# Kernel optimization log

Hardware: AMD Instinct MI355X
Metric: run time of the kernel (lower is better)

Reference implementation:

```python
import jax, jax.numpy as jnp
import numpy as np

N = 4096      # nodes
F = 512       # nfeat
D = 64        # nhid per head
H = 8         # nheads
C = 40        # nclass
ALPHA = 0.2   # leakyrelu slope
NEG = -1e9    # mask value (finite for bf16/fp16 safety; exp -> 0)
EDGE_P = 0.004


def setup_inputs() -> dict:
    key = jax.random.key(0)
    ks = jax.random.split(key, 8)
    x = jax.random.normal(ks[0], (N, F), jnp.float32)
    adj = jax.random.uniform(ks[1], (N, N)) < EDGE_P
    adj = adj | jnp.eye(N, dtype=bool)  # self-loops: every softmax row valid
    init = lambda k, shape, fan: jax.random.normal(k, shape, jnp.float32) / np.sqrt(fan)
    W1 = init(ks[2], (H, F, D), F)        # per-head tran.weight^T
    a1_src = init(ks[3], (H, D), D)       # att1 (j / source term)
    a1_dst = init(ks[4], (H, D), D)       # att2 (i / destination term)
    W2 = init(ks[5], (H * D, C), H * D)   # output head tran
    a2_src = init(ks[6], (C,), C)
    a2_dst = init(ks[7], (C,), C)
    return dict(x=x, adj=adj, W1=W1, a1_src=a1_src, a1_dst=a1_dst,
                W2=W2, a2_src=a2_src, a2_dst=a2_dst)


def reference(x, adj, W1, a1_src, a1_dst, W2, a2_src, a2_dst):
    # ---- layer 1: H heads in parallel (dropout = identity in eval) ----
    h = jnp.einsum('nf,hfd->hnd', x, W1)              # [H,N,D]
    si = jnp.einsum('hnd,hd->hn', h, a1_dst)          # att2(h): i term
    sj = jnp.einsum('hnd,hd->hn', h, a1_src)          # att1(h): j term
    e = jax.nn.leaky_relu(si[:, :, None] + sj[:, None, :], ALPHA)  # [H,N,N]
    e = jnp.where(adj[None], e, NEG)                  # mask non-edges
    p = jax.nn.softmax(e, axis=-1)                    # softmax over neighbors j
    out = jnp.einsum('hij,hjd->hid', p, h)            # [H,N,D]
    # torch.cat(heads, dim=1) -> [N, H*D] with heads contiguous
    x2 = jax.nn.elu(jnp.transpose(out, (1, 0, 2)).reshape(N, H * D))
    # ---- output attention head ----
    h2 = x2 @ W2                                      # [N,C]
    e2 = jax.nn.leaky_relu((h2 @ a2_dst)[:, None] + (h2 @ a2_src)[None, :], ALPHA)
    e2 = jnp.where(adj, e2, NEG)
    p2 = jax.nn.softmax(e2, axis=-1)
    return p2 @ h2                                    # [N,C]
```

## Files before the change

kernel.cpp:

```cpp
#include <hip/hip_runtime.h>

#define NN 4096
#define FF 512
#define DD 64
#define HH 8
#define CC 40
#define HD (HH * DD)
#define CP 64
#define MAXDEG 128
#define ALPHA 0.2f

#define BM 64
#define BN 64
#define BK 16
#define SK 2
#define KH (FF / SK)
#define SK2 8
#define KH2 (FF / SK2)

__device__ __forceinline__ float bf2f(unsigned short u) {
    union { unsigned int i; float f; } v;
    v.i = ((unsigned int)u) << 16;
    return v.f;
}

__device__ __forceinline__ float wave_sum(float v) {
    #pragma unroll
    for (int off = 32; off; off >>= 1) v += __shfl_xor(v, off, 64);
    return v;
}

__device__ __forceinline__ float wave_max(float v) {
    #pragma unroll
    for (int off = 32; off; off >>= 1) v = fmaxf(v, __shfl_xor(v, off, 64));
    return v;
}

__device__ __forceinline__ float read_f(const void* src, int i, int isBf16) {
    if (isBf16) return bf2f(((const unsigned short*)src)[i]);
    return ((const float*)src)[i];
}

__global__ __launch_bounds__(64) void init_flags(int* __restrict__ flagA,
                                                 int* __restrict__ flagF) {
    if (threadIdx.x == 0) { *flagA = 1; *flagF = 1; }
}

__global__ __launch_bounds__(64) void sniff_adj(const unsigned char* __restrict__ adj,
                                                int* __restrict__ flagA) {
    int i = blockIdx.x * 64 + threadIdx.x;
    if (adj[(size_t)i * (NN + 1)] == 0) *flagA = 0;
}

__global__ __launch_bounds__(256) void sniff_fdt(const unsigned int* __restrict__ xw,
                                                 int* __restrict__ flagF) {
    int bad = 0;
    #pragma unroll
    for (int q = 0; q < 4; q++) {
        unsigned int w = xw[(blockIdx.x * 4 + q) * 256 + threadIdx.x];
        unsigned int e0 = (w >> 7) & 0xffu;
        unsigned int e1 = (w >> 23) & 0xffu;
        if (e0 >= 0x90u || e1 >= 0x90u) bad = 1;
    }
    if (bad) *flagF = 0;
}

__global__ __launch_bounds__(256) void cvt_all(const void* __restrict__ x,
                                               const void* __restrict__ W1,
                                               const void* __restrict__ W2,
                                               const void* __restrict__ a1s,
                                               const void* __restrict__ a1d,
                                               const void* __restrict__ a2s,
                                               const void* __restrict__ a2d,
                                               float* __restrict__ xf,
                                               float* __restrict__ W1t,
                                               float* __restrict__ W2p,
                                               float* __restrict__ a1sf,
                                               float* __restrict__ a1df,
                                               float* __restrict__ a2sf,
                                               float* __restrict__ a2df,
                                               const int* __restrict__ flagF) {
    int i = blockIdx.x * 256 + threadIdx.x;
    int bf = *flagF;
    const int nX = NN * FF;
    const int nW1 = HH * FF * DD;
    const int nW2p = HD * CP;
    const int nA1 = HD;
    if (i < nX) { xf[i] = read_f(x, i, bf); return; }
    i -= nX;
    if (i < nW1) {
        int hd = i / (FF * DD);
        int rem = i % (FF * DD);
        int f = rem / DD, d = rem % DD;
        W1t[f * HD + hd * DD + d] = read_f(W1, i, bf);
        return;
    }
    i -= nW1;
    if (i < nW2p) {
        int k = i / CP, c = i % CP;
        W2p[i] = (c < CC) ? read_f(W2, k * CC + c, bf) : 0.f;
        return;
    }
    i -= nW2p;
    if (i < nA1) { a1sf[i] = read_f(a1s, i, bf); return; }
    i -= nA1;
    if (i < nA1) { a1df[i] = read_f(a1d, i, bf); return; }
    i -= nA1;
    if (i < CC) { a2sf[i] = read_f(a2s, i, bf); return; }
    i -= CC;
    if (i < CC) { a2df[i] = read_f(a2d, i, bf); return; }
}

__global__ __launch_bounds__(256) void build_nbr(const unsigned char* __restrict__ adj,
                                                 const int* __restrict__ flagA,
                                                 int* __restrict__ nbr,
                                                 int* __restrict__ deg) {
    int i = blockIdx.x;
    __shared__ int cnt;
    if (threadIdx.x == 0) cnt = 0;
    __syncthreads();
    if (*flagA) {
        uint4 v = ((const uint4*)(adj + (size_t)i * NN))[threadIdx.x];
        unsigned int u[4] = { v.x, v.y, v.z, v.w };
        int base = threadIdx.x * 16;
        #pragma unroll
        for (int q = 0; q < 4; q++) {
            #pragma unroll
            for (int b = 0; b < 4; b++) {
                if ((u[q] >> (8 * b)) & 0xffu) {
                    int p = atomicAdd(&cnt, 1);
                    if (p < MAXDEG) nbr[(size_t)i * MAXDEG + p] = base + q * 4 + b;
                }
            }
        }
    } else {
        const int4* row = (const int4*)((const int*)adj + (size_t)i * NN);
        #pragma unroll
        for (int q = 0; q < 4; q++) {
            int idx4 = q * 256 + threadIdx.x;
            int4 v = row[idx4];
            int base = idx4 * 4;
            if (v.x) { int p = atomicAdd(&cnt, 1); if (p < MAXDEG) nbr[(size_t)i * MAXDEG + p] = base; }
            if (v.y) { int p = atomicAdd(&cnt, 1); if (p < MAXDEG) nbr[(size_t)i * MAXDEG + p] = base + 1; }
            if (v.z) { int p = atomicAdd(&cnt, 1); if (p < MAXDEG) nbr[(size_t)i * MAXDEG + p] = base + 2; }
            if (v.w) { int p = atomicAdd(&cnt, 1); if (p < MAXDEG) nbr[(size_t)i * MAXDEG + p] = base + 3; }
        }
    }
    __syncthreads();
    if (threadIdx.x == 0) deg[i] = min(cnt, MAXDEG);
}

template <int KHs, int Nb>
__device__ __forceinline__ void gemm_body(const float* __restrict__ Ap,
                                          const float* __restrict__ Bp,
                                          float* __restrict__ Co,
                                          int tid, int bm) {
    __shared__ float As[BK][BM + 4];
    __shared__ float Bs[BK][BN + 4];
    int tm = tid >> 4, tn = tid & 15;
    int m0 = tm * 4, n0 = tn * 4;
    int ar = tid >> 2, ak = (tid & 3) * 4;
    int bk = tid >> 4, bq = (tid & 15) * 4;

    float acc[4][4];
    #pragma unroll
    for (int r = 0; r < 4; r++)
        #pragma unroll
        for (int c = 0; c < 4; c++) acc[r][c] = 0.f;

    const float* Ar = Ap + (size_t)ar * FF;
    float4 av = *(const float4*)(Ar + ak);
    float4 bv = *(const float4*)(Bp + (size_t)bk * Nb + bq);

    for (int k0 = 0; k0 < KHs; k0 += BK) {
        __syncthreads();
        As[ak + 0][ar] = av.x;
        As[ak + 1][ar] = av.y;
        As[ak + 2][ar] = av.z;
        As[ak + 3][ar] = av.w;
        *(float4*)&Bs[bk][bq] = bv;
        __syncthreads();

        int kn = (k0 + BK < KHs) ? k0 + BK : k0;
        av = *(const float4*)(Ar + kn + ak);
        bv = *(const float4*)(Bp + (size_t)(kn + bk) * Nb + bq);

        #pragma unroll
        for (int k = 0; k < BK; k++) {
            float4 a = *(const float4*)&As[k][m0];
            float4 b = *(const float4*)&Bs[k][n0];
            acc[0][0] = fmaf(a.x, b.x, acc[0][0]);
            acc[0][1] = fmaf(a.x, b.y, acc[0][1]);
            acc[0][2] = fmaf(a.x, b.z, acc[0][2]);
            acc[0][3] = fmaf(a.x, b.w, acc[0][3]);
            acc[1][0] = fmaf(a.y, b.x, acc[1][0]);
            acc[1][1] = fmaf(a.y, b.y, acc[1][1]);
            acc[1][2] = fmaf(a.y, b.z, acc[1][2]);
            acc[1][3] = fmaf(a.y, b.w, acc[1][3]);
            acc[2][0] = fmaf(a.z, b.x, acc[2][0]);
            acc[2][1] = fmaf(a.z, b.y, acc[2][1]);
            acc[2][2] = fmaf(a.z, b.z, acc[2][2]);
            acc[2][3] = fmaf(a.z, b.w, acc[2][3]);
            acc[3][0] = fmaf(a.w, b.x, acc[3][0]);
            acc[3][1] = fmaf(a.w, b.y, acc[3][1]);
            acc[3][2] = fmaf(a.w, b.z, acc[3][2]);
            acc[3][3] = fmaf(a.w, b.w, acc[3][3]);
        }
    }

    #pragma unroll
    for (int r = 0; r < 4; r++) {
        float4 v = make_float4(acc[r][0], acc[r][1], acc[r][2], acc[r][3]);
        *(float4*)(Co + (size_t)(bm * BM + m0 + r) * Nb + n0) = v;
    }
}

__global__ __launch_bounds__(256) void l1_gemm(const float* __restrict__ xf,
                                               const float* __restrict__ W1t,
                                               float* __restrict__ Cp) {
    int bm = blockIdx.x, bn = blockIdx.y, sk = blockIdx.z;
    gemm_body<KH, HD>(xf + (size_t)bm * BM * FF + sk * KH,
                      W1t + (size_t)(sk * KH) * HD + bn * BN,
                      Cp + (size_t)sk * NN * HD + bn * BN,
                      threadIdx.x, bm);
}

__global__ __launch_bounds__(256) void l1_post(const float* __restrict__ Cp,
                                               const float* __restrict__ a1sf,
                                               const float* __restrict__ a1df,
                                               float* __restrict__ h,
                                               float* __restrict__ si,
                                               float* __restrict__ sj) {
    int n = blockIdx.x, tid = threadIdx.x;
    #pragma unroll
    for (int q = 0; q < 2; q++) {
        int t = q * 256 + tid;
        float v = Cp[(size_t)n * HD + t] + Cp[(size_t)NN * HD + (size_t)n * HD + t];
        h[(size_t)n * HD + t] = v;
        int hd = t >> 6;
        float pd = wave_sum(v * a1df[t]);
        float ps = wave_sum(v * a1sf[t]);
        if ((t & 63) == 0) {
            si[hd * NN + n] = pd;
            sj[hd * NN + n] = ps;
        }
    }
}

__global__ __launch_bounds__(512) void l1_attn(const int* __restrict__ nbr,
                                               const int* __restrict__ deg,
                                               const float* __restrict__ h,
                                               const float* __restrict__ si,
                                               const float* __restrict__ sj,
                                               float* __restrict__ x2) {
    int i = blockIdx.x;
    int tid = threadIdx.x;
    int hd = tid >> 6, lane = tid & 63;
    int d = deg[i];
    __shared__ int js[MAXDEG];
    __shared__ float wls[HH][MAXDEG];
    for (int k = tid; k < d; k += 512) js[k] = nbr[(size_t)i * MAXDEG + k];
    __syncthreads();

    float sii = si[hd * NN + i];
    const float* sjh = sj + (size_t)hd * NN;
    float m = -1e30f;
    for (int k = lane; k < d; k += 64) {
        float sc = sii + sjh[js[k]];
        sc = sc > 0.f ? sc : ALPHA * sc;
        wls[hd][k] = sc;
        m = fmaxf(m, sc);
    }
    m = wave_max(m);
    float s = 0.f;
    for (int k = lane; k < d; k += 64) {
        float e = expf(wls[hd][k] - m);
        wls[hd][k] = e;
        s += e;
    }
    s = fmaxf(wave_sum(s), 1e-30f);

    float acc = 0.f;
    int k = 0;
    for (; k + 4 <= d; k += 4) {
        float v0 = h[(size_t)js[k] * HD + tid];
        float v1 = h[(size_t)js[k + 1] * HD + tid];
        float v2 = h[(size_t)js[k + 2] * HD + tid];
        float v3 = h[(size_t)js[k + 3] * HD + tid];
        acc = fmaf(wls[hd][k], v0, acc);
        acc = fmaf(wls[hd][k + 1], v1, acc);
        acc = fmaf(wls[hd][k + 2], v2, acc);
        acc = fmaf(wls[hd][k + 3], v3, acc);
    }
    for (; k < d; k++)
        acc = fmaf(wls[hd][k], h[(size_t)js[k] * HD + tid], acc);
    acc /= s;
    float r = acc > 0.f ? acc : expm1f(acc);
    x2[(size_t)i * HD + tid] = r;
}

__global__ __launch_bounds__(256) void l2_gemm(const float* __restrict__ x2,
                                               const float* __restrict__ W2p,
                                               float* __restrict__ Cp2) {
    int bm = blockIdx.x, sk = blockIdx.z;
    gemm_body<KH2, CP>(x2 + (size_t)bm * BM * FF + sk * KH2,
                       W2p + (size_t)(sk * KH2) * CP,
                       Cp2 + (size_t)sk * NN * CP,
                       threadIdx.x, bm);
}

__global__ __launch_bounds__(64) void l2_post(const float* __restrict__ Cp2,
                                              const float* __restrict__ a2sf,
                                              const float* __restrict__ a2df,
                                              float* __restrict__ h2,
                                              float* __restrict__ d1,
                                              float* __restrict__ d2) {
    int n = blockIdx.x, c = threadIdx.x;
    float v = 0.f;
    #pragma unroll
    for (int sk = 0; sk < SK2; sk++)
        v += Cp2[(size_t)sk * NN * CP + (size_t)n * CP + c];
    if (c < CC) h2[(size_t)n * CC + c] = v;
    float pd = wave_sum((c < CC) ? v * a2df[c] : 0.f);
    float ps = wave_sum((c < CC) ? v * a2sf[c] : 0.f);
    if (c == 0) {
        d1[n] = pd;
        d2[n] = ps;
    }
}

__global__ __launch_bounds__(256) void l2_attn(const int* __restrict__ nbr,
                                               const int* __restrict__ deg,
                                               const float* __restrict__ h2,
                                               const float* __restrict__ d1,
                                               const float* __restrict__ d2,
                                               float* __restrict__ out) {
    int w = threadIdx.x >> 6, lane = threadIdx.x & 63;
    int i = blockIdx.x * 4 + w;
    int d = deg[i];
    __shared__ int js[4][MAXDEG];
    __shared__ float wls[4][MAXDEG];
    for (int k = lane; k < d; k += 64) js[w][k] = nbr[(size_t)i * MAXDEG + k];

    float sii = d1[i];
    float m = -1e30f;
    for (int k = lane; k < d; k += 64) {
        float sc = sii + d2[js[w][k]];
        sc = sc > 0.f ? sc : ALPHA * sc;
        wls[w][k] = sc;
        m = fmaxf(m, sc);
    }
    m = wave_max(m);
    float s = 0.f;
    for (int k = lane; k < d; k += 64) {
        float e = expf(wls[w][k] - m);
        wls[w][k] = e;
        s += e;
    }
    s = fmaxf(wave_sum(s), 1e-30f);

    int c = lane;
    if (c < CC) {
        float acc = 0.f;
        int k = 0;
        for (; k + 4 <= d; k += 4) {
            float v0 = h2[(size_t)js[w][k] * CC + c];
            float v1 = h2[(size_t)js[w][k + 1] * CC + c];
            float v2 = h2[(size_t)js[w][k + 2] * CC + c];
            float v3 = h2[(size_t)js[w][k + 3] * CC + c];
            acc = fmaf(wls[w][k], v0, acc);
            acc = fmaf(wls[w][k + 1], v1, acc);
            acc = fmaf(wls[w][k + 2], v2, acc);
            acc = fmaf(wls[w][k + 3], v3, acc);
        }
        for (; k < d; k++)
            acc = fmaf(wls[w][k], h2[(size_t)js[w][k] * CC + c], acc);
        out[(size_t)i * CC + c] = acc / s;
    }
}

extern "C" void kernel_launch(void* const* d_in, const int* in_sizes, int n_in,
                              void* d_out, int out_size, void* d_ws, size_t ws_size,
                              hipStream_t stream) {
    const void* x   = d_in[0];
    const unsigned char* adj = (const unsigned char*)d_in[1];
    const void* W1  = d_in[2];
    const void* a1s = d_in[3];
    const void* a1d = d_in[4];
    const void* W2  = d_in[5];
    const void* a2s = d_in[6];
    const void* a2d = d_in[7];

    char* ws = (char*)d_ws;
    int*   nbr  = (int*)(ws + 0);
    int*   deg  = (int*)(ws + 2097152);
    float* si   = (float*)(ws + 10502144);
    float* sj   = (float*)(ws + 10633216);
    float* xf   = (float*)(ws + 10764288);
    float* x2   = (float*)(ws + 10764288);
    float* h2   = (float*)(ws + 19152896);
    float* d1   = (float*)(ws + 19808256);
    float* d2   = (float*)(ws + 19824640);
    int*   flagA= (int*)(ws + 19841024);
    int*   flagF= (int*)(ws + 19841028);
    float* W1t  = (float*)(ws + 19841040);
    float* a1sf = (float*)(ws + 20889616);
    float* a1df = (float*)(ws + 20891664);
    float* W2p  = (float*)(ws + 20893712);
    float* a2sf = (float*)(ws + 21024784);
    float* a2df = (float*)(ws + 21024944);
    float* CpBase = (float*)(ws + 21025104);
    float* h    = CpBase;
    float* Cp2  = CpBase + (size_t)NN * HD;

    hipLaunchKernelGGL(init_flags, dim3(1), dim3(64), 0, stream, flagA, flagF);
    hipLaunchKernelGGL(sniff_adj, dim3(NN / 64), dim3(64), 0, stream, adj, flagA);
    hipLaunchKernelGGL(sniff_fdt, dim3(64), dim3(256), 0, stream,
                       (const unsigned int*)x, flagF);

    const int nCvt = NN * FF + HH * FF * DD + HD * CP + 2 * HD + 2 * CC;
    hipLaunchKernelGGL(cvt_all, dim3((nCvt + 255) / 256), dim3(256), 0, stream,
                       x, W1, W2, a1s, a1d, a2s, a2d,
                       xf, W1t, W2p, a1sf, a1df, a2sf, a2df, flagF);

    hipLaunchKernelGGL(build_nbr, dim3(NN), dim3(256), 0, stream, adj, flagA, nbr, deg);
    hipLaunchKernelGGL(l1_gemm, dim3(NN / BM, HD / BN, SK), dim3(256), 0, stream,
                       xf, W1t, CpBase);
    hipLaunchKernelGGL(l1_post, dim3(NN), dim3(256), 0, stream,
                       CpBase, a1sf, a1df, h, si, sj);
    hipLaunchKernelGGL(l1_attn, dim3(NN), dim3(512), 0, stream,
                       nbr, deg, h, si, sj, x2);
    hipLaunchKernelGGL(l2_gemm, dim3(NN / BM, 1, SK2), dim3(256), 0, stream,
                       x2, W2p, Cp2);
    hipLaunchKernelGGL(l2_post, dim3(NN), dim3(64), 0, stream,
                       Cp2, a2sf, a2df, h2, d1, d2);
    hipLaunchKernelGGL(l2_attn, dim3(NN / 4), dim3(256), 0, stream,
                       nbr, deg, h2, d1, d2, (float*)d_out);
}
```

Measured before the change: 198.4 us.

## Fuse layer-1 GEMM with attention-score epilogue, drop split-K and merge sniff kernels

Layer-1 GEMM now runs over the full K dimension with one block per head tile and computes the si/sj attention dot products in its epilogue via shuffles, removing the split-K partial buffer and the separate l1_post kernel. The fp32 path reads x directly instead of copying it into xf, and the two sniff kernels are merged into one launch. The attention aggregation loop is also unrolled by 8. The trade-off is half as many GEMM blocks, each with a longer K loop, in exchange for fewer launches and less intermediate traffic.

```diff
diff --git a/kernel.cpp b/kernel.cpp
--- a/kernel.cpp
+++ b/kernel.cpp
@@ -13,8 +13,6 @@
 #define BM 64
 #define BN 64
 #define BK 16
-#define SK 2
-#define KH (FF / SK)
 #define SK2 8
 #define KH2 (FF / SK2)
 
@@ -46,23 +44,26 @@
     if (threadIdx.x == 0) { *flagA = 1; *flagF = 1; }
 }
 
-__global__ __launch_bounds__(64) void sniff_adj(const unsigned char* __restrict__ adj,
-                                                int* __restrict__ flagA) {
-    int i = blockIdx.x * 64 + threadIdx.x;
-    if (adj[(size_t)i * (NN + 1)] == 0) *flagA = 0;
-}
-
-__global__ __launch_bounds__(256) void sniff_fdt(const unsigned int* __restrict__ xw,
-                                                 int* __restrict__ flagF) {
-    int bad = 0;
-    #pragma unroll
-    for (int q = 0; q < 4; q++) {
-        unsigned int w = xw[(blockIdx.x * 4 + q) * 256 + threadIdx.x];
-        unsigned int e0 = (w >> 7) & 0xffu;
-        unsigned int e1 = (w >> 23) & 0xffu;
-        if (e0 >= 0x90u || e1 >= 0x90u) bad = 1;
-    }
-    if (bad) *flagF = 0;
+__global__ __launch_bounds__(256) void sniff_both(const unsigned char* __restrict__ adj,
+                                                  const unsigned int* __restrict__ xw,
+                                                  int* __restrict__ flagA,
+                                                  int* __restrict__ flagF) {
+    int b = blockIdx.x;
+    if (b < 16) {
+        int i = b * 256 + threadIdx.x;
+        if (adj[(size_t)i * (NN + 1)] == 0) *flagA = 0;
+    } else {
+        int bb = b - 16;
+        int bad = 0;
+        #pragma unroll
+        for (int q = 0; q < 4; q++) {
+            unsigned int w = xw[(bb * 4 + q) * 256 + threadIdx.x];
+            unsigned int e0 = (w >> 7) & 0xffu;
+            unsigned int e1 = (w >> 23) & 0xffu;
+            if (e0 >= 0x90u || e1 >= 0x90u) bad = 1;
+        }
+        if (bad) *flagF = 0;
+    }
 }
 
 __global__ __launch_bounds__(256) void cvt_all(const void* __restrict__ x,
@@ -86,7 +87,10 @@
     const int nW1 = HH * FF * DD;
     const int nW2p = HD * CP;
     const int nA1 = HD;
-    if (i < nX) { xf[i] = read_f(x, i, bf); return; }
+    if (i < nX) {
+        if (bf) xf[i] = bf2f(((const unsigned short*)x)[i]);
+        return;
+    }
     i -= nX;
     if (i < nW1) {
         int hd = i / (FF * DD);
@@ -150,11 +154,18 @@
     if (threadIdx.x == 0) deg[i] = min(cnt, MAXDEG);
 }
 
-template <int KHs, int Nb>
-__device__ __forceinline__ void gemm_body(const float* __restrict__ Ap,
-                                          const float* __restrict__ Bp,
-                                          float* __restrict__ Co,
-                                          int tid, int bm) {
+__global__ __launch_bounds__(256) void l1_gemm(const void* __restrict__ xraw,
+                                               const float* __restrict__ xf,
+                                               const float* __restrict__ W1t,
+                                               const float* __restrict__ a1sf,
+                                               const float* __restrict__ a1df,
+                                               const int* __restrict__ flagF,
+                                               float* __restrict__ h,
+                                               float* __restrict__ si,
+                                               float* __restrict__ sj) {
+    const float* A = *flagF ? xf : (const float*)xraw;
+    int bm = blockIdx.x, hd = blockIdx.y;
+    int tid = threadIdx.x;
     __shared__ float As[BK][BM + 4];
     __shared__ float Bs[BK][BN + 4];
     int tm = tid >> 4, tn = tid & 15;
@@ -162,17 +173,19 @@
     int ar = tid >> 2, ak = (tid & 3) * 4;
     int bk = tid >> 4, bq = (tid & 15) * 4;
 
+    const float* Ar = A + (size_t)(bm * BM + ar) * FF;
+    const float* Bp = W1t + (size_t)hd * BN;
+
     float acc[4][4];
     #pragma unroll
     for (int r = 0; r < 4; r++)
         #pragma unroll
         for (int c = 0; c < 4; c++) acc[r][c] = 0.f;
 
-    const float* Ar = Ap + (size_t)ar * FF;
     float4 av = *(const float4*)(Ar + ak);
-    float4 bv = *(const float4*)(Bp + (size_t)bk * Nb + bq);
-
-    for (int k0 = 0; k0 < KHs; k0 += BK) {
+    float4 bv = *(const float4*)(Bp + (size_t)bk * HD + bq);
+
+    for (int k0 = 0; k0 < FF; k0 += BK) {
         __syncthreads();
         As[ak + 0][ar] = av.x;
         As[ak + 1][ar] = av.y;
@@ -181,9 +194,9 @@
         *(float4*)&Bs[bk][bq] = bv;
         __syncthreads();
 
-        int kn = (k0 + BK < KHs) ? k0 + BK : k0;
+        int kn = (k0 + BK < FF) ? k0 + BK : k0;
         av = *(const float4*)(Ar + kn + ak);
-        bv = *(const float4*)(Bp + (size_t)(kn + bk) * Nb + bq);
+        bv = *(const float4*)(Bp + (size_t)(kn + bk) * HD + bq);
 
         #pragma unroll
         for (int k = 0; k < BK; k++) {
@@ -208,41 +221,29 @@
         }
     }
 
+    float ad[4], asr[4];
+    #pragma unroll
+    for (int q = 0; q < 4; q++) {
+        ad[q] = a1df[hd * DD + n0 + q];
+        asr[q] = a1sf[hd * DD + n0 + q];
+    }
     #pragma unroll
     for (int r = 0; r < 4; r++) {
+        int row = bm * BM + m0 + r;
         float4 v = make_float4(acc[r][0], acc[r][1], acc[r][2], acc[r][3]);
-        *(float4*)(Co + (size_t)(bm * BM + m0 + r) * Nb + n0) = v;
-    }
-}
-
-__global__ __launch_bounds__(256) void l1_gemm(const float* __restrict__ xf,
-                                               const float* __restrict__ W1t,
-                                               float* __restrict__ Cp) {
-    int bm = blockIdx.x, bn = blockIdx.y, sk = blockIdx.z;
-    gemm_body<KH, HD>(xf + (size_t)bm * BM * FF + sk * KH,
-                      W1t + (size_t)(sk * KH) * HD + bn * BN,
-                      Cp + (size_t)sk * NN * HD + bn * BN,
-                      threadIdx.x, bm);
-}
-
-__global__ __launch_bounds__(256) void l1_post(const float* __restrict__ Cp,
-                                               const float* __restrict__ a1sf,
-                                               const float* __restrict__ a1df,
-                                               float* __restrict__ h,
-                                               float* __restrict__ si,
-                                               float* __restrict__ sj) {
-    int n = blockIdx.x, tid = threadIdx.x;
-    #pragma unroll
-    for (int q = 0; q < 2; q++) {
-        int t = q * 256 + tid;
-        float v = Cp[(size_t)n * HD + t] + Cp[(size_t)NN * HD + (size_t)n * HD + t];
-        h[(size_t)n * HD + t] = v;
-        int hd = t >> 6;
-        float pd = wave_sum(v * a1df[t]);
-        float ps = wave_sum(v * a1sf[t]);
-        if ((t & 63) == 0) {
-            si[hd * NN + n] = pd;
-            sj[hd * NN + n] = ps;
+        *(float4*)(h + (size_t)row * HD + hd * DD + n0) = v;
+        float pd = acc[r][0] * ad[0] + acc[r][1] * ad[1]
+                 + acc[r][2] * ad[2] + acc[r][3] * ad[3];
+        float ps = acc[r][0] * asr[0] + acc[r][1] * asr[1]
+                 + acc[r][2] * asr[2] + acc[r][3] * asr[3];
+        #pragma unroll
+        for (int off = 1; off < 16; off <<= 1) {
+            pd += __shfl_xor(pd, off, 64);
+            ps += __shfl_xor(ps, off, 64);
+        }
+        if (tn == 0) {
+            si[hd * NN + row] = pd;
+            sj[hd * NN + row] = ps;
         }
     }
 }
@@ -282,6 +283,24 @@
 
     float acc = 0.f;
     int k = 0;
+    for (; k + 8 <= d; k += 8) {
+        float v0 = h[(size_t)js[k] * HD + tid];
+        float v1 = h[(size_t)js[k + 1] * HD + tid];
+        float v2 = h[(size_t)js[k + 2] * HD + tid];
+        float v3 = h[(size_t)js[k + 3] * HD + tid];
+        float v4 = h[(size_t)js[k + 4] * HD + tid];
+        float v5 = h[(size_t)js[k + 5] * HD + tid];
+        float v6 = h[(size_t)js[k + 6] * HD + tid];
+        float v7 = h[(size_t)js[k + 7] * HD + tid];
+        acc = fmaf(wls[hd][k], v0, acc);
+        acc = fmaf(wls[hd][k + 1], v1, acc);
+        acc = fmaf(wls[hd][k + 2], v2, acc);
+        acc = fmaf(wls[hd][k + 3], v3, acc);
+        acc = fmaf(wls[hd][k + 4], v4, acc);
+        acc = fmaf(wls[hd][k + 5], v5, acc);
+        acc = fmaf(wls[hd][k + 6], v6, acc);
+        acc = fmaf(wls[hd][k + 7], v7, acc);
+    }
     for (; k + 4 <= d; k += 4) {
         float v0 = h[(size_t)js[k] * HD + tid];
         float v1 = h[(size_t)js[k + 1] * HD + tid];
@@ -297,6 +316,71 @@
     acc /= s;
     float r = acc > 0.f ? acc : expm1f(acc);
     x2[(size_t)i * HD + tid] = r;
+}
+
+template <int KHs, int Nb>
+__device__ __forceinline__ void gemm_body(const float* __restrict__ Ap,
+                                          const float* __restrict__ Bp,
+                                          float* __restrict__ Co,
+                                          int tid, int bm) {
+    __shared__ float As[BK][BM + 4];
+    __shared__ float Bs[BK][BN + 4];
+    int tm = tid >> 4, tn = tid & 15;
+    int m0 = tm * 4, n0 = tn * 4;
+    int ar = tid >> 2, ak = (tid & 3) * 4;
+    int bk = tid >> 4, bq = (tid & 15) * 4;
+
+    float acc[4][4];
+    #pragma unroll
+    for (int r = 0; r < 4; r++)
+        #pragma unroll
+        for (int c = 0; c < 4; c++) acc[r][c] = 0.f;
+
+    const float* Ar = Ap + (size_t)ar * FF;
+    float4 av = *(const float4*)(Ar + ak);
+    float4 bv = *(const float4*)(Bp + (size_t)bk * Nb + bq);
+
+    for (int k0 = 0; k0 < KHs; k0 += BK) {
+        __syncthreads();
+        As[ak + 0][ar] = av.x;
+        As[ak + 1][ar] = av.y;
+        As[ak + 2][ar] = av.z;
+        As[ak + 3][ar] = av.w;
+        *(float4*)&Bs[bk][bq] = bv;
+        __syncthreads();
+
+        int kn = (k0 + BK < KHs) ? k0 + BK : k0;
+        av = *(const float4*)(Ar + kn + ak);
+        bv = *(const float4*)(Bp + (size_t)(kn + bk) * Nb + bq);
+
+        #pragma unroll
+        for (int k = 0; k < BK; k++) {
+            float4 a = *(const float4*)&As[k][m0];
+            float4 b = *(const float4*)&Bs[k][n0];
+            acc[0][0] = fmaf(a.x, b.x, acc[0][0]);
+            acc[0][1] = fmaf(a.x, b.y, acc[0][1]);
+            acc[0][2] = fmaf(a.x, b.z, acc[0][2]);
+            acc[0][3] = fmaf(a.x, b.w, acc[0][3]);
+            acc[1][0] = fmaf(a.y, b.x, acc[1][0]);
+            acc[1][1] = fmaf(a.y, b.y, acc[1][1]);
+            acc[1][2] = fmaf(a.y, b.z, acc[1][2]);
+            acc[1][3] = fmaf(a.y, b.w, acc[1][3]);
+            acc[2][0] = fmaf(a.z, b.x, acc[2][0]);
+            acc[2][1] = fmaf(a.z, b.y, acc[2][1]);
+            acc[2][2] = fmaf(a.z, b.z, acc[2][2]);
+            acc[2][3] = fmaf(a.z, b.w, acc[2][3]);
+            acc[3][0] = fmaf(a.w, b.x, acc[3][0]);
+            acc[3][1] = fmaf(a.w, b.y, acc[3][1]);
+            acc[3][2] = fmaf(a.w, b.z, acc[3][2]);
+            acc[3][3] = fmaf(a.w, b.w, acc[3][3]);
+        }
+    }
+
+    #pragma unroll
+    for (int r = 0; r < 4; r++) {
+        float4 v = make_float4(acc[r][0], acc[r][1], acc[r][2], acc[r][3]);
+        *(float4*)(Co + (size_t)(bm * BM + m0 + r) * Nb + n0) = v;
+    }
 }
 
 __global__ __launch_bounds__(256) void l2_gemm(const float* __restrict__ x2,
@@ -409,14 +493,12 @@
     float* W2p  = (float*)(ws + 20893712);
     float* a2sf = (float*)(ws + 21024784);
     float* a2df = (float*)(ws + 21024944);
-    float* CpBase = (float*)(ws + 21025104);
-    float* h    = CpBase;
-    float* Cp2  = CpBase + (size_t)NN * HD;
+    float* h    = (float*)(ws + 21025104);
+    float* Cp2  = h + (size_t)NN * HD;
 
     hipLaunchKernelGGL(init_flags, dim3(1), dim3(64), 0, stream, flagA, flagF);
-    hipLaunchKernelGGL(sniff_adj, dim3(NN / 64), dim3(64), 0, stream, adj, flagA);
-    hipLaunchKernelGGL(sniff_fdt, dim3(64), dim3(256), 0, stream,
-                       (const unsigned int*)x, flagF);
+    hipLaunchKernelGGL(sniff_both, dim3(80), dim3(256), 0, stream,
+                       adj, (const unsigned int*)x, flagA, flagF);
 
     const int nCvt = NN * FF + HH * FF * DD + HD * CP + 2 * HD + 2 * CC;
     hipLaunchKernelGGL(cvt_all, dim3((nCvt + 255) / 256), dim3(256), 0, stream,
@@ -424,10 +506,8 @@
                        xf, W1t, W2p, a1sf, a1df, a2sf, a2df, flagF);
 
     hipLaunchKernelGGL(build_nbr, dim3(NN), dim3(256), 0, stream, adj, flagA, nbr, deg);
-    hipLaunchKernelGGL(l1_gemm, dim3(NN / BM, HD / BN, SK), dim3(256), 0, stream,
-                       xf, W1t, CpBase);
-    hipLaunchKernelGGL(l1_post, dim3(NN), dim3(256), 0, stream,
-                       CpBase, a1sf, a1df, h, si, sj);
+    hipLaunchKernelGGL(l1_gemm, dim3(NN / BM, HH), dim3(256), 0, stream,
+                       x, xf, W1t, a1sf, a1df, flagF, h, si, sj);
     hipLaunchKernelGGL(l1_attn, dim3(NN), dim3(512), 0, stream,
                        nbr, deg, h, si, sj, x2);
     hipLaunchKernelGGL(l2_gemm, dim3(NN / BM, 1, SK2), dim3(256), 0, stream,
```

Measured after the change: 188.4 us. 1.05x faster.
